# Kernel tuning notes

Hardware: AMD Instinct MI355X
Metric: run time of the kernel (lower is better)

Reference implementation:

```python
import jax, jax.numpy as jnp
import numpy as np

B = 1024          # batch of positions
K = 64            # king squares
F = 640           # 64 squares * 10 piece types
C = 256           # accumulator channels


def setup_inputs() -> dict:
    key = jax.random.key(0)
    k1, k2, k3 = jax.random.split(key, 3)
    piece_positions = jax.random.randint(k1, (B, 64, 10), 0, 2).astype(jnp.bool_)
    king_positions = jax.random.randint(k2, (B, 2), 0, K, dtype=jnp.int32)
    input_weights = jax.random.normal(k3, (K, F + 1, C), dtype=jnp.float32)
    bias = jnp.zeros((C,), dtype=jnp.float32)
    return {
        "piece_positions": piece_positions,
        "king_positions": king_positions,
        "input_weights": input_weights,
        "bias": bias,
    }


def reference(piece_positions, king_positions, input_weights, bias):
    # Flatten the (64, 10) boolean piece plane into 640 HalfKP features.
    b = piece_positions.shape[0]
    p = piece_positions.reshape(b, F).astype(input_weights.dtype)          # (B, 640)
    # Gather each sample's white/black king weight slabs: (B, 2, 641, 256)
    Wg = jnp.take(input_weights, king_positions, axis=0)
    # Sparse-feature sum for both halves, contracted over feature dim and
    # summed over the two king perspectives in one einsum.
    halves = jnp.einsum("bf,bsfc->bc", p, Wg[:, :, :F, :])                 # (B, 256)
    extra = Wg[:, :, F, :].sum(axis=1)                                     # row 640 for each king
    return halves + extra + bias
```

## Files before the change

### kernel.cpp

```cpp
#include <hip/hip_runtime.h>
#include <hip/hip_bf16.h>


#define F_DIM 640
#define C_DIM 256
#define SLAB_STRIDE (641 * 256)
#define NKING 64
#define LCAP 256
#define NC_MAX 64

#define WS_MASK_OFF 0
#define WS_PART_OFF 81920
#define WS_NEED (WS_PART_OFF + 2 * 1024 * 256 * 4)

typedef float  f32x4  __attribute__((ext_vector_type(4)));
typedef short  bf16x8 __attribute__((ext_vector_type(8)));

__device__ __forceinline__ unsigned f2bf_pk(float a, float b) {
    union { float f; unsigned u; } x, y;
    x.f = a; y.f = b;
    const unsigned ra = (x.u + 0x7FFFu + ((x.u >> 16) & 1u)) >> 16;
    const unsigned rb = (y.u + 0x7FFFu + ((y.u >> 16) & 1u)) >> 16;
    return (ra & 0xFFFFu) | (rb << 16);
}

__device__ __forceinline__ bf16x8 mk_a8(unsigned m32, int g) {
    const unsigned by = (m32 >> (g * 8)) & 0xFFu;
    union { unsigned u[4]; bf16x8 v; } r;
    #pragma unroll
    for (int i = 0; i < 4; ++i)
        r.u[i] = (((by >> (2 * i)) & 1u) ? 0x3F80u : 0u) |
                 (((by >> (2 * i + 1)) & 1u) ? 0x3F800000u : 0u);
    return r.v;
}

__global__ __launch_bounds__(256)
void pack_masks(const int* __restrict__ pieces,
                unsigned long long* __restrict__ mask,
                int nwords)
{
    const int gw = blockIdx.x * 4 + (threadIdx.x >> 6);
    const int lane = threadIdx.x & 63;
    if (gw >= nwords) return;
    const int v = pieces[(size_t)gw * 64 + lane];
    const unsigned long long m = __ballot(v != 0);
    if (lane == 0) mask[gw] = m;
}

__global__ __launch_bounds__(512, 4)
void halfkp_mfma(const float* __restrict__ W,
                 const unsigned long long* __restrict__ mask,
                 const int* __restrict__ kings,
                 float* __restrict__ partial,
                 int nent)
{
    const int k  = blockIdx.x;
    const int cq = blockIdx.y;
    const int t  = threadIdx.x;
    const int wv = t >> 6, lane = t & 63;
    const int mt = wv & 3, ntc = wv >> 2;
    const int li = lane & 15, g = lane >> 4;
    const int col = cq * 32 + ntc * 16 + li;

    __shared__ int s_ent[LCAP];
    __shared__ int s_cb[NC_MAX + 1];
    __shared__ unsigned s_m32[64][21];
    __shared__ int s_nk;

    const int NC = nent >> 6;
    const int nit = NC >> 3;
    unsigned long long mm[8];
    #pragma unroll
    for (int it = 0; it < 8; ++it) {
        if (it < nit) {
            const int c = wv + (it << 3);
            const int kk = kings[(c << 6) + lane];
            mm[it] = __ballot(kk == k);
            if (lane == 0) s_cb[c] = (int)__popcll(mm[it]);
        }
    }
    __syncthreads();
    if (t == 0) {
        int s = 0;
        for (int c = 0; c < NC; ++c) { const int v = s_cb[c]; s_cb[c] = s; s += v; }
        s_cb[NC] = s;
        s_nk = min(s, LCAP);
    }
    __syncthreads();
    const unsigned long long lt = (1ull << lane) - 1ull;
    #pragma unroll
    for (int it = 0; it < 8; ++it) {
        if (it < nit) {
            const int c = wv + (it << 3);
            if ((mm[it] >> lane) & 1ull) {
                const int pos = s_cb[c] + (int)__popcll(mm[it] & lt);
                if (pos < LCAP) s_ent[pos] = (c << 6) + lane;
            }
        }
    }
    __syncthreads();
    const int n_k = s_nk;

    const float* __restrict__ Wk = W + (size_t)k * SLAB_STRIDE;
    const float* __restrict__ Wc = Wk + col;

    for (int mb = 0; mb < n_k; mb += 64) {
        const int nc = min(n_k - mb, 64);

        for (int idx = t; idx < 64 * 21; idx += 512) {
            const int row = idx & 63, ks = idx >> 6;
            const int id = (row < nc) ? s_ent[mb + row] : -1;
            unsigned v = 0;
            if (id >= 0) {
                if (ks < 20) {
                    const unsigned long long mw = mask[(size_t)(id >> 1) * 10 + (ks >> 1)];
                    v = (unsigned)(mw >> ((ks & 1) * 32));
                } else {
                    v = 1u;
                }
            }
            s_m32[row][ks] = v;
        }
        __syncthreads();

        f32x4 acc = {0.f, 0.f, 0.f, 0.f};
        #pragma unroll 3
        for (int ks = 0; ks < 21; ++ks) {
            float wt[8];
            #pragma unroll
            for (int j = 0; j < 8; ++j) {
                const int f = min(ks * 32 + g * 8 + j, F_DIM);
                wt[j] = Wc[(size_t)f * C_DIM];
            }
            union { unsigned u[4]; bf16x8 v; } bb;
            #pragma unroll
            for (int j = 0; j < 4; ++j)
                bb.u[j] = f2bf_pk(wt[2 * j], wt[2 * j + 1]);
            const bf16x8 af = mk_a8(s_m32[mt * 16 + li][ks], g);
            acc = __builtin_amdgcn_mfma_f32_16x16x32_bf16(af, bb.v, acc, 0, 0, 0);
        }

        #pragma unroll
        for (int i = 0; i < 4; ++i) {
            const int row = mt * 16 + 4 * g + i;
            if (row < nc) {
                const int id = s_ent[mb + row];
                partial[(((size_t)(id & 1)) * 1024 + (id >> 1)) * C_DIM + col] = acc[i];
            }
        }
        __syncthreads();
    }
}

__global__ __launch_bounds__(256)
void finalize(const float* __restrict__ partial,
              const float* __restrict__ bias,
              float* __restrict__ out)
{
    const int i = blockIdx.x * 256 + threadIdx.x;
    const float4 b4 = ((const float4*)bias)[i & 63];
    const float4 p0 = ((const float4*)partial)[i];
    const float4 p1 = ((const float4*)partial)[1024 * 64 + i];
    float4 o;
    o.x = b4.x + p0.x + p1.x;
    o.y = b4.y + p0.y + p1.y;
    o.z = b4.z + p0.z + p1.z;
    o.w = b4.w + p0.w + p1.w;
    ((float4*)out)[i] = o;
}

__global__ __launch_bounds__(256)
void halfkp_fallback(const int* __restrict__ pieces, const int* __restrict__ kings,
                     const float* __restrict__ W, const float* __restrict__ bias,
                     float* __restrict__ out)
{
    const int b = blockIdx.x;
    const int c = threadIdx.x;
    const int lane = c & 63;
    const int k0 = kings[2 * b + 0];
    const int k1 = kings[2 * b + 1];
    const float* W0 = W + (size_t)k0 * SLAB_STRIDE + c;
    const float* W1 = W + (size_t)k1 * SLAB_STRIDE + c;
    float acc = bias[c] + W0[640 * 256] + W1[640 * 256];
    const int* pi = pieces + (size_t)b * F_DIM;
    #pragma unroll
    for (int ch = 0; ch < 10; ++ch) {
        int v = pi[ch * 64 + lane];
        unsigned long long m = __ballot(v != 0);
        const float* b0 = W0 + ch * 64 * 256;
        const float* b1 = W1 + ch * 64 * 256;
        while (m) {
            const int f = __builtin_ctzll(m);
            m &= m - 1;
            acc += b0[f * 256] + b1[f * 256];
        }
    }
    out[(size_t)b * C_DIM + c] = acc;
}

extern "C" void kernel_launch(void* const* d_in, const int* in_sizes, int n_in,
                              void* d_out, int out_size, void* d_ws, size_t ws_size,
                              hipStream_t stream) {
    const int* pieces = (const int*)d_in[0];
    const int* kings  = (const int*)d_in[1];
    const float* W    = (const float*)d_in[2];
    const float* bias = (const float*)d_in[3];
    float* out        = (float*)d_out;

    const int B = in_sizes[1] / 2;
    const int nent = 2 * B;
    const int nwords = B * 10;

    if (ws_size < (size_t)WS_NEED) {
        halfkp_fallback<<<dim3(B), dim3(C_DIM), 0, stream>>>(pieces, kings, W, bias, out);
        return;
    }

    unsigned long long* mask = (unsigned long long*)((char*)d_ws + WS_MASK_OFF);
    float* part = (float*)((char*)d_ws + WS_PART_OFF);

    pack_masks<<<dim3((nwords + 3) / 4), dim3(256), 0, stream>>>(pieces, mask, nwords);
    halfkp_mfma<<<dim3(NKING, 8), dim3(512), 0, stream>>>(W, mask, kings, part, nent);
    finalize<<<dim3(B * 64 / 256), dim3(256), 0, stream>>>(part, bias, out);
}
```

Baseline: 27.43 us.

## Stage bf16 weight slab in LDS and split K across waves with reduction

Each block now loads its king's weight slice for 16 columns once with float4 loads, converts it to packed bf16 pairs and stores it in padded shared memory. The load is issued before the king-list compaction so its latency overlaps that work. Previously every wave re-read strided scalar global weights for each entry tile. The MFMA loop is split across four waves along the feature (K) dimension, and partial accumulators are reduced through shared memory. The grid doubles to 16 column slices per king and the occupancy hint rises. In exchange, the extra barriers and the LDS reduction add synchronisation per tile.

Result: no change. 27.45 us (+0.1%).

```diff
diff --git a/kernel.cpp b/kernel.cpp
--- a/kernel.cpp
+++ b/kernel.cpp
@@ -8,6 +8,7 @@
 #define NKING 64
 #define LCAP 256
 #define NC_MAX 64
+#define WPAD 20
 
 #define WS_MASK_OFF 0
 #define WS_PART_OFF 81920
@@ -47,7 +48,7 @@
     if (lane == 0) mask[gw] = m;
 }
 
-__global__ __launch_bounds__(512, 4)
+__global__ __launch_bounds__(512, 8)
 void halfkp_mfma(const float* __restrict__ W,
                  const unsigned long long* __restrict__ mask,
                  const int* __restrict__ kings,
@@ -58,58 +59,87 @@
     const int cq = blockIdx.y;
     const int t  = threadIdx.x;
     const int wv = t >> 6, lane = t & 63;
-    const int mt = wv & 3, ntc = wv >> 2;
+    const int mt = wv & 1;
+    const int kh = wv >> 1;
     const int li = lane & 15, g = lane >> 4;
-    const int col = cq * 32 + ntc * 16 + li;
-
+    const int colG = cq * 16 + li;
+
+    __shared__ unsigned s_W[336 * WPAD];
     __shared__ int s_ent[LCAP];
     __shared__ int s_cb[NC_MAX + 1];
     __shared__ unsigned s_m32[64][21];
+    __shared__ f32x4 s_red[4][64];
     __shared__ int s_nk;
 
-    const int NC = nent >> 6;
-    const int nit = NC >> 3;
-    unsigned long long mm[8];
-    #pragma unroll
-    for (int it = 0; it < 8; ++it) {
-        if (it < nit) {
-            const int c = wv + (it << 3);
-            const int kk = kings[(c << 6) + lane];
-            mm[it] = __ballot(kk == k);
-            if (lane == 0) s_cb[c] = (int)__popcll(mm[it]);
-        }
-    }
-    __syncthreads();
-    if (t == 0) {
-        int s = 0;
-        for (int c = 0; c < NC; ++c) { const int v = s_cb[c]; s_cb[c] = s; s += v; }
-        s_cb[NC] = s;
-        s_nk = min(s, LCAP);
-    }
-    __syncthreads();
-    const unsigned long long lt = (1ull << lane) - 1ull;
-    #pragma unroll
-    for (int it = 0; it < 8; ++it) {
-        if (it < nit) {
-            const int c = wv + (it << 3);
-            if ((mm[it] >> lane) & 1ull) {
-                const int pos = s_cb[c] + (int)__popcll(mm[it] & lt);
-                if (pos < LCAP) s_ent[pos] = (c << 6) + lane;
-            }
+    const float* __restrict__ Wq = W + (size_t)k * SLAB_STRIDE + cq * 16;
+    float4 ve[3], vo[3];
+    #pragma unroll
+    for (int it = 0; it < 3; ++it) {
+        const int task = t + (it << 9);
+        if (task < 336 * 4) {
+            const int fp = task >> 2, c4 = task & 3;
+            const int fe = min(2 * fp, F_DIM);
+            const int fo = min(2 * fp + 1, F_DIM);
+            ve[it] = *(const float4*)&Wq[(size_t)fe * C_DIM + c4 * 4];
+            vo[it] = *(const float4*)&Wq[(size_t)fo * C_DIM + c4 * 4];
+        }
+    }
+
+    {
+        const int NC = nent >> 6;
+        const int nit = NC >> 3;
+        unsigned long long mm[8];
+        #pragma unroll
+        for (int it = 0; it < 8; ++it) {
+            if (it < nit) {
+                const int c = wv + (it << 3);
+                const int kk = kings[(c << 6) + lane];
+                mm[it] = __ballot(kk == k);
+                if (lane == 0) s_cb[c] = (int)__popcll(mm[it]);
+            }
+        }
+        __syncthreads();
+        if (t == 0) {
+            int s = 0;
+            for (int c = 0; c < NC; ++c) { const int v = s_cb[c]; s_cb[c] = s; s += v; }
+            s_nk = min(s, LCAP);
+        }
+        __syncthreads();
+        const unsigned long long lt = (1ull << lane) - 1ull;
+        #pragma unroll
+        for (int it = 0; it < 8; ++it) {
+            if (it < nit) {
+                const int c = wv + (it << 3);
+                if ((mm[it] >> lane) & 1ull) {
+                    const int pos = s_cb[c] + (int)__popcll(mm[it] & lt);
+                    if (pos < LCAP) s_ent[pos] = (c << 6) + lane;
+                }
+            }
+        }
+    }
+
+    #pragma unroll
+    for (int it = 0; it < 3; ++it) {
+        const int task = t + (it << 9);
+        if (task < 336 * 4) {
+            const int fp = task >> 2, c4 = task & 3;
+            union { unsigned u[4]; f32x4 v; } pk;
+            pk.u[0] = f2bf_pk(ve[it].x, vo[it].x);
+            pk.u[1] = f2bf_pk(ve[it].y, vo[it].y);
+            pk.u[2] = f2bf_pk(ve[it].z, vo[it].z);
+            pk.u[3] = f2bf_pk(ve[it].w, vo[it].w);
+            *(f32x4*)&s_W[fp * WPAD + c4 * 4] = pk.v;
         }
     }
     __syncthreads();
     const int n_k = s_nk;
 
-    const float* __restrict__ Wk = W + (size_t)k * SLAB_STRIDE;
-    const float* __restrict__ Wc = Wk + col;
-
     for (int mb = 0; mb < n_k; mb += 64) {
-        const int nc = min(n_k - mb, 64);
+        const int ncc = min(n_k - mb, 64);
 
         for (int idx = t; idx < 64 * 21; idx += 512) {
             const int row = idx & 63, ks = idx >> 6;
-            const int id = (row < nc) ? s_ent[mb + row] : -1;
+            const int id = (row < ncc) ? s_ent[mb + row] : -1;
             unsigned v = 0;
             if (id >= 0) {
                 if (ks < 20) {
@@ -123,30 +153,46 @@
         }
         __syncthreads();
 
-        f32x4 acc = {0.f, 0.f, 0.f, 0.f};
-        #pragma unroll 3
-        for (int ks = 0; ks < 21; ++ks) {
-            float wt[8];
-            #pragma unroll
-            for (int j = 0; j < 8; ++j) {
-                const int f = min(ks * 32 + g * 8 + j, F_DIM);
-                wt[j] = Wc[(size_t)f * C_DIM];
-            }
-            union { unsigned u[4]; bf16x8 v; } bb;
-            #pragma unroll
-            for (int j = 0; j < 4; ++j)
-                bb.u[j] = f2bf_pk(wt[2 * j], wt[2 * j + 1]);
-            const bf16x8 af = mk_a8(s_m32[mt * 16 + li][ks], g);
-            acc = __builtin_amdgcn_mfma_f32_16x16x32_bf16(af, bb.v, acc, 0, 0, 0);
-        }
-
-        #pragma unroll
-        for (int i = 0; i < 4; ++i) {
-            const int row = mt * 16 + 4 * g + i;
-            if (row < nc) {
-                const int id = s_ent[mb + row];
-                partial[(((size_t)(id & 1)) * 1024 + (id >> 1)) * C_DIM + col] = acc[i];
-            }
+        const int ntiles = (ncc + 15) >> 4;
+        const int ks_beg = (kh == 0) ? 0 : (kh == 1) ? 6 : (kh == 2) ? 11 : 16;
+        const int ks_end = (kh == 0) ? 6 : (kh == 1) ? 11 : (kh == 2) ? 16 : 21;
+
+        for (int tb = 0; tb < ntiles; tb += 2) {
+            const int tile = tb + mt;
+            const bool live = tile * 16 < ncc;
+            f32x4 acc = {0.f, 0.f, 0.f, 0.f};
+            if (live) {
+                const unsigned* mrow = s_m32[tile * 16 + li];
+                #pragma unroll 2
+                for (int ks = ks_beg; ks < ks_end; ++ks) {
+                    const unsigned* bp = &s_W[(ks * 16 + g * 4) * WPAD + li];
+                    union { unsigned u[4]; bf16x8 v; } bb;
+                    #pragma unroll
+                    for (int jj = 0; jj < 4; ++jj)
+                        bb.u[jj] = bp[jj * WPAD];
+                    const bf16x8 af = mk_a8(mrow[ks], g);
+                    acc = __builtin_amdgcn_mfma_f32_16x16x32_bf16(af, bb.v, acc, 0, 0, 0);
+                }
+                if (kh >= 2) s_red[mt * 2 + kh - 2][lane] = acc;
+            }
+            __syncthreads();
+            if (live && kh < 2) {
+                acc += s_red[mt * 2 + kh][lane];
+                if (kh == 1) s_red[mt * 2][lane] = acc;
+            }
+            __syncthreads();
+            if (live && kh == 0) {
+                acc += s_red[mt * 2][lane];
+                #pragma unroll
+                for (int i = 0; i < 4; ++i) {
+                    const int r = tile * 16 + 4 * g + i;
+                    if (r < ncc) {
+                        const int id = s_ent[mb + r];
+                        partial[(((size_t)(id & 1)) * 1024 + (id >> 1)) * C_DIM + colG] = acc[i];
+                    }
+                }
+            }
+            __syncthreads();
         }
         __syncthreads();
     }
@@ -220,6 +266,6 @@
     float* part = (float*)((char*)d_ws + WS_PART_OFF);
 
     pack_masks<<<dim3((nwords + 3) / 4), dim3(256), 0, stream>>>(pieces, mask, nwords);
-    halfkp_mfma<<<dim3(NKING, 8), dim3(512), 0, stream>>>(W, mask, kings, part, nent);
+    halfkp_mfma<<<dim3(NKING, 16), dim3(512), 0, stream>>>(W, mask, kings, part, nent);
     finalize<<<dim3(B * 64 / 256), dim3(256), 0, stream>>>(part, bias, out);
 }
```
